# Performance work log

Hardware: AMD Instinct MI355X
Metric: run time of the kernel (lower is better)

The kernel has to match this reference:

```python
import jax, jax.numpy as jnp
import numpy as np

N_HEADS = 12
NEG_INF = -1e9


def rotate_half(x):
    x1, x2 = jnp.split(x, 2, axis=-1)
    return jnp.concatenate((-x2, x1), axis=-1)


def rope_tables(T, D, dtype):
    # matches RotaryEmbedding buffers: emb = cat(freqs, freqs), shape [1,1,T,D]
    inv_freq = 1.0 / (10000.0 ** (jnp.arange(0, D, 2, dtype=jnp.float32) / D))
    t = jnp.arange(T, dtype=jnp.float32)
    freqs = jnp.einsum('i,j->ij', t, inv_freq)
    emb = jnp.concatenate((freqs, freqs), axis=-1)
    return jnp.cos(emb)[None, None].astype(dtype), jnp.sin(emb)[None, None].astype(dtype)


def setup_inputs() -> dict:
    key = jax.random.key(0)
    ks = jax.random.split(key, 5)
    B, T, C = 4, 2048, 768
    s = 1.0 / np.sqrt(C)
    x = jax.random.normal(ks[0], (B, T, C), dtype=jnp.float32)
    wq = jax.random.normal(ks[1], (C, C), dtype=jnp.float32) * s
    wk = jax.random.normal(ks[2], (C, C), dtype=jnp.float32) * s
    wv = jax.random.normal(ks[3], (C, C), dtype=jnp.float32) * s
    wo = jax.random.normal(ks[4], (C, C), dtype=jnp.float32) * s
    causal = jnp.tril(jnp.ones((T, T), dtype=bool))
    mask = jnp.where(causal, 0.0, NEG_INF).astype(jnp.float32)[None, None]
    return {"x": x, "wq": wq, "wk": wk, "wv": wv, "wo": wo, "mask": mask}


def reference(x, wq, wk, wv, wo, mask):
    B, T, C = x.shape
    H = N_HEADS
    D = C // H
    # QKV projections (no bias), reshape to [B,H,T,D]
    def proj(w):
        return (x @ w).reshape(B, T, H, D).transpose(0, 2, 1, 3)
    q, k, v = proj(wq), proj(wk), proj(wv)
    cos, sin = rope_tables(T, D, x.dtype)
    q = q * cos + rotate_half(q) * sin
    k = k * cos + rotate_half(k) * sin
    attn = jnp.einsum('bhqd,bhkd->bhqk', q, k) / jnp.sqrt(jnp.asarray(D, x.dtype))
    attn = attn + mask
    attn = jax.nn.softmax(attn, axis=-1)  # dropout = identity (eval mode)
    out = jnp.einsum('bhqk,bhkd->bhqd', attn, v)
    out = out.transpose(0, 2, 1, 3).reshape(B, T, C)
    return out @ wo
```

## Files before the change

kernel.cpp:

```cpp
#include <hip/hip_runtime.h>
#include <hip/hip_bf16.h>
#include <cmath>

typedef _Float16 f16x8 __attribute__((ext_vector_type(8)));
typedef float f32x4 __attribute__((ext_vector_type(4)));

#define T_SEQ 2048
#define C_DIM 768
#define H_NUM 12
#define NX (8192 * 768)
#define NW (768 * 768)

__device__ __forceinline__ unsigned short f2h(float f) {
    _Float16 h = (_Float16)f;
    return __builtin_bit_cast(unsigned short, h);
}

__device__ __forceinline__ float fexp2(float x) {
#if __has_builtin(__builtin_amdgcn_exp2f)
    return __builtin_amdgcn_exp2f(x);
#else
    return exp2f(x);
#endif
}

__device__ __forceinline__ unsigned int pkrtz(float a, float b) {
    auto r = __builtin_amdgcn_cvt_pkrtz(a, b);
    return __builtin_bit_cast(unsigned int, r);
}

__device__ __forceinline__ unsigned int permlo(unsigned int d0, unsigned int d1) {
#if __has_builtin(__builtin_amdgcn_perm)
    return __builtin_amdgcn_perm(d1, d0, 0x05040100u);
#else
    return (d0 & 0xffffu) | (d1 << 16);
#endif
}
__device__ __forceinline__ unsigned int permhi(unsigned int d0, unsigned int d1) {
#if __has_builtin(__builtin_amdgcn_perm)
    return __builtin_amdgcn_perm(d1, d0, 0x07060302u);
#else
    return (d0 >> 16) | (d1 & 0xffff0000u);
#endif
}

__device__ __forceinline__ void gld16(const unsigned short* g, unsigned short* l) {
    __builtin_amdgcn_global_load_lds(
        (const __attribute__((address_space(1))) unsigned int*)g,
        (__attribute__((address_space(3))) unsigned int*)l, 16, 0, 0);
}

__global__ __launch_bounds__(256)
void prep(const float* __restrict__ x,
          const float* __restrict__ w0, const float* __restrict__ w1,
          const float* __restrict__ w2, const float* __restrict__ w3,
          unsigned short* __restrict__ xb, unsigned short* __restrict__ wt) {
    __shared__ float T[64][65];
    const int pid = blockIdx.x;
    if (pid < 3072) {
        int cidx = pid * 256 + threadIdx.x;
        int row = cidx / 96;
        int cp = cidx - row * 96;
        int dchunk = row * 96 + (cp & ~3) + ((cp & 3) ^ (row & 3));
        const float* s = x + (size_t)cidx * 8;
        float4 v0 = *(const float4*)s, v1 = *(const float4*)(s + 4);
        ushort4 a, b;
        a.x = f2h(v0.x); a.y = f2h(v0.y); a.z = f2h(v0.z); a.w = f2h(v0.w);
        b.x = f2h(v1.x); b.y = f2h(v1.y); b.z = f2h(v1.z); b.w = f2h(v1.w);
        unsigned short* d = xb + (size_t)dchunk * 8;
        *(ushort4*)d = a;
        *(ushort4*)(d + 4) = b;
    } else {
        int t = pid - 3072;
        int z = t / 144, r = t - z * 144;
        int kx = r / 12, ny = r - kx * 12;
        const float* src = (z == 0) ? w0 : (z == 1) ? w1 : (z == 2) ? w2 : w3;
        unsigned short* dst = wt + (size_t)z * NW;
        const int k0 = kx * 64, n0 = ny * 64;
        const int tid = threadIdx.x;
        {
            int rowb = tid >> 4, c4 = (tid & 15) * 4;
#pragma unroll
            for (int i = 0; i < 4; ++i) {
                int row = rowb + i * 16;
                float4 v = *(const float4*)&src[(size_t)(k0 + row) * C_DIM + n0 + c4];
                T[row][c4] = v.x; T[row][c4 + 1] = v.y; T[row][c4 + 2] = v.z; T[row][c4 + 3] = v.w;
            }
        }
        __syncthreads();
        {
            int n = tid & 63, kseg = (tid >> 6) * 16;
            int n_glob = n0 + n;
            unsigned short tmp[16];
#pragma unroll
            for (int j = 0; j < 16; ++j) tmp[j] = f2h(T[kseg + j][n]);
            int base = k0 + (kseg & 32);
            int sub = (kseg >> 3) & 3;
            unsigned short* drow = dst + (size_t)n_glob * C_DIM + base;
            *(uint4*)&drow[(sub ^ (n_glob & 3)) << 3]       = *(uint4*)&tmp[0];
            *(uint4*)&drow[((sub + 1) ^ (n_glob & 3)) << 3] = *(uint4*)&tmp[8];
        }
    }
}

__global__ __launch_bounds__(256, 4)
void qkv_gemm(const unsigned short* __restrict__ xb,
              const unsigned short* __restrict__ wt,
              unsigned short* __restrict__ q_ws,
              unsigned short* __restrict__ k_ws,
              unsigned short* __restrict__ vt_ws) {
    const int pid = blockIdx.x;
    const int xcd = pid & 7, idx = pid >> 3;
    const int mloc = idx / 18, nw = idx - mloc * 18;
    const int which = nw % 3, nx = nw / 3;
    const unsigned short* W = wt + (size_t)which * NW;
    const int n0 = nx * 128, m0 = (xcd * 8 + mloc) * 128;

    __shared__ __align__(16) unsigned short As[8192];
    __shared__ __align__(16) unsigned short Bs[8192];

    const int tid = threadIdx.x, lane = tid & 63, w = tid >> 6;
    const int quad = lane >> 4, l16 = lane & 15;
    const int wm = (w >> 1) * 64, wn = (w & 1) * 64;

    f32x4 acc[4][4] = {};

    for (int k0 = 0; k0 < C_DIM; k0 += 64) {
        __syncthreads();
#pragma unroll
        for (int c = 0; c < 4; ++c) {
            int e = c * 256 + tid;
            int p = e >> 9, row = (e >> 2) & 127, ch = e & 3;
            int kc = k0 + p * 32 + ch * 8;
            gld16(xb + (size_t)(m0 + row) * C_DIM + kc, &As[e * 8]);
            gld16(W  + (size_t)(n0 + row) * C_DIM + kc, &Bs[e * 8]);
        }
        __syncthreads();
#pragma unroll
        for (int p = 0; p < 2; ++p) {
            f16x8 af[4], bf[4];
#pragma unroll
            for (int mt = 0; mt < 4; ++mt) {
                int r = wm + mt * 16 + l16;
                af[mt] = *(const f16x8*)&As[p * 4096 + r * 32 + ((quad ^ (r & 3)) << 3)];
            }
#pragma unroll
            for (int nt = 0; nt < 4; ++nt) {
                int r = wn + nt * 16 + l16;
                bf[nt] = *(const f16x8*)&Bs[p * 4096 + r * 32 + ((quad ^ (r & 3)) << 3)];
            }
#pragma unroll
            for (int mt = 0; mt < 4; ++mt)
#pragma unroll
                for (int nt = 0; nt < 4; ++nt)
                    acc[mt][nt] = __builtin_amdgcn_mfma_f32_16x16x32_f16(af[mt], bf[nt], acc[mt][nt], 0, 0, 0);
        }
    }

    const int head = nx * 2 + (w & 1);

    if (which < 2) {
        unsigned short* dst = (which == 0) ? q_ws : k_ws;
        const float qscale = 0.18033688011112042f;
#pragma unroll
        for (int ntp = 0; ntp < 2; ++ntp) {
            int d1 = ntp * 16 + l16;
            float invf = __expf(-0.28782313662425572f * (float)d1);
#pragma unroll
            for (int mt = 0; mt < 4; ++mt)
#pragma unroll
                for (int reg = 0; reg < 4; ++reg) {
                    int m = m0 + wm + mt * 16 + quad * 4 + reg;
                    int t = m & (T_SEQ - 1), bb = m >> 11;
                    float sn, cs;
                    __sincosf((float)t * invf, &sn, &cs);
                    float v1 = acc[mt][ntp][reg], v2 = acc[mt][ntp + 2][reg];
                    float o1 = v1 * cs - v2 * sn;
                    float o2 = v2 * cs + v1 * sn;
                    if (which == 0) { o1 *= qscale; o2 *= qscale; }
                    size_t o = ((size_t)(bb * H_NUM + head) * T_SEQ + t) * 64 + d1;
                    dst[o] = f2h(o1);
                    dst[o + 32] = f2h(o2);
                }
        }
    } else {
#pragma unroll
        for (int nt = 0; nt < 4; ++nt) {
            int d = nt * 16 + l16;
#pragma unroll
            for (int mt = 0; mt < 4; ++mt) {
                int m = m0 + wm + mt * 16 + quad * 4;
                int t = m & (T_SEQ - 1), bb = m >> 11;
                ushort4 pk;
                pk.x = f2h(acc[mt][nt][0]); pk.y = f2h(acc[mt][nt][1]);
                pk.z = f2h(acc[mt][nt][2]); pk.w = f2h(acc[mt][nt][3]);
                *(ushort4*)&vt_ws[((size_t)(bb * H_NUM + head) * 64 + d) * T_SEQ + t] = pk;
            }
        }
    }
}

__global__ __launch_bounds__(256, 3)
void flash_attn(const unsigned short* __restrict__ q_ws,
                const unsigned short* __restrict__ k_ws,
                const unsigned short* __restrict__ vt_ws,
                unsigned short* __restrict__ attn_out) {
    __shared__ __align__(16) unsigned short Kbuf[2][64 * 64];
    __shared__ __align__(16) unsigned int Ps32[4][16 * 64];

    const int pid = blockIdx.x;
    const int xcd = pid & 7, slot = pid >> 3;
    const int bh_l = slot >> 4;
    const int bh = xcd * 6 + bh_l;
    const int pr = (slot + 3 * bh_l) & 15;
    const int qa = pr, qb = 31 - pr;
    const int b = bh / H_NUM, h = bh % H_NUM;

    const int tid = threadIdx.x, lane = tid & 63, w = tid >> 6;
    const int quad = lane >> 4, l16 = lane & 15;
    const size_t base = (size_t)bh * (T_SEQ * 64);

    const unsigned short* qAp = q_ws + base + (size_t)(qa * 64 + w * 16 + l16) * 64 + quad * 8;
    f16x8 aqA0 = *(const f16x8*)(qAp);
    f16x8 aqA1 = *(const f16x8*)(qAp + 32);
    const unsigned short* qBp = q_ws + base + (size_t)(qb * 64 + w * 16 + l16) * 64 + quad * 8;
    f16x8 aqB0 = *(const f16x8*)(qBp);
    f16x8 aqB1 = *(const f16x8*)(qBp + 32);

    f32x4 accA[4] = {}, accB[4] = {};
    f32x4 laccA = {}, laccB = {};
    f16x8 onesf;
#pragma unroll
    for (int i = 0; i < 8; ++i) onesf[i] = (_Float16)1.0f;

    unsigned int* pw = &Ps32[w][0];

    const int r_in = lane >> 3;
    const int cpr = lane & 7;
    const int gch = (cpr ^ r_in) * 8;

#define DMA_K(P, KT)                                                                   \
    {                                                                                  \
        _Pragma("unroll")                                                              \
        for (int j = 0; j < 2; ++j) {                                                  \
            int row = w * 16 + j * 8 + r_in;                                           \
            gld16(k_ws + base + (size_t)((KT) * 64 + row) * 64 + gch,                  \
                  &Kbuf[P][(w * 16 + j * 8) * 64]);                                    \
        }                                                                              \
    }

    const int fo = (quad ^ (l16 & 7)) << 3;

    const unsigned short* vrow = vt_ws + base + (size_t)l16 * T_SEQ + quad * 8;

    const int wg = (quad & 1) * 4;
    const int l16q = l16 >> 2, l16m = l16 & 3;
    const int s7 = l16 & 7;
    const int rA = l16 * 64;
    const int rp0a = rA + (((2 * quad) ^ s7) << 2);
    const int rp0b = rA + (((2 * quad + 1) ^ s7) << 2);

    DMA_K(0, 0);
    for (int kt = 0; kt <= qb; ++kt) {
        const int cur = kt & 1;
        __syncthreads();
        if (kt < qb) DMA_K(cur ^ 1, kt + 1);
        const int doA = (kt <= qa);

        f16x8 bv[4][2];
#pragma unroll
        for (int nt = 0; nt < 4; ++nt) {
            const unsigned short* vp = vrow + (size_t)nt * 16 * T_SEQ + kt * 64;
            bv[nt][0] = *(const f16x8*)(vp);
            bv[nt][1] = *(const f16x8*)(vp + 32);
        }

        f16x8 bk[4][2];
#pragma unroll
        for (int nt = 0; nt < 4; ++nt) {
            const unsigned short* kr = &Kbuf[cur][(nt * 16 + l16) * 64 + fo];
            bk[nt][0] = *(const f16x8*)(kr);
            bk[nt][1] = *(const f16x8*)((const unsigned short*)((size_t)kr ^ 64));
        }

        f32x4 sB[4] = {}, sA[4] = {};
        __builtin_amdgcn_s_setprio(1);
#pragma unroll
        for (int nt = 0; nt < 4; ++nt) {
            sB[nt] = __builtin_amdgcn_mfma_f32_16x16x32_f16(aqB0, bk[nt][0], sB[nt], 0, 0, 0);
            sB[nt] = __builtin_amdgcn_mfma_f32_16x16x32_f16(aqB1, bk[nt][1], sB[nt], 0, 0, 0);
        }
        if (doA) {
#pragma unroll
            for (int nt = 0; nt < 4; ++nt) {
                sA[nt] = __builtin_amdgcn_mfma_f32_16x16x32_f16(aqA0, bk[nt][0], sA[nt], 0, 0, 0);
                sA[nt] = __builtin_amdgcn_mfma_f32_16x16x32_f16(aqA1, bk[nt][1], sA[nt], 0, 0, 0);
            }
        }
        __builtin_amdgcn_s_setprio(0);
        if (kt == qb) {
#pragma unroll
            for (int nt = 0; nt < 4; ++nt)
#pragma unroll
                for (int reg = 0; reg < 4; ++reg)
                    if (nt * 16 + l16 > w * 16 + quad * 4 + reg) sB[nt][reg] = -1e30f;
        }
        if (kt == qa) {
#pragma unroll
            for (int nt = 0; nt < 4; ++nt)
#pragma unroll
                for (int reg = 0; reg < 4; ++reg)
                    if (nt * 16 + l16 > w * 16 + quad * 4 + reg) sA[nt][reg] = -1e30f;
        }

        if (doA) {
#pragma unroll
            for (int nt = 0; nt < 4; ++nt)
#pragma unroll
                for (int reg = 0; reg < 4; ++reg) {
                    float pB = fexp2(sB[nt][reg]);
                    float pA = fexp2(sA[nt][reg]);
                    pw[(quad * 4 + reg) * 64 + ((((nt * 4) | l16q) ^ (wg | reg)) << 2) + l16m] = pkrtz(pB, pA);
                }
        } else {
#pragma unroll
            for (int nt = 0; nt < 4; ++nt)
#pragma unroll
                for (int reg = 0; reg < 4; ++reg) {
                    float pB = fexp2(sB[nt][reg]);
                    pw[(quad * 4 + reg) * 64 + ((((nt * 4) | l16q) ^ (wg | reg)) << 2) + l16m] = pkrtz(pB, pB);
                }
        }

        uint4 c0 = *(const uint4*)(pw + rp0a);
        uint4 c1 = *(const uint4*)(pw + rp0b);
        uint4 c2 = *(const uint4*)(pw + rp0a + 32);
        uint4 c3 = *(const uint4*)(pw + rp0b + 32);

        uint4 lo0 = { permlo(c0.x, c0.y), permlo(c0.z, c0.w), permlo(c1.x, c1.y), permlo(c1.z, c1.w) };
        uint4 lo1 = { permlo(c2.x, c2.y), permlo(c2.z, c2.w), permlo(c3.x, c3.y), permlo(c3.z, c3.w) };
        f16x8 apB0 = __builtin_bit_cast(f16x8, lo0);
        f16x8 apB1 = __builtin_bit_cast(f16x8, lo1);
        __builtin_amdgcn_s_setprio(1);
#pragma unroll
        for (int nt = 0; nt < 4; ++nt) {
            accB[nt] = __builtin_amdgcn_mfma_f32_16x16x32_f16(apB0, bv[nt][0], accB[nt], 0, 0, 0);
            accB[nt] = __builtin_amdgcn_mfma_f32_16x16x32_f16(apB1, bv[nt][1], accB[nt], 0, 0, 0);
        }
        laccB = __builtin_amdgcn_mfma_f32_16x16x32_f16(apB0, onesf, laccB, 0, 0, 0);
        laccB = __builtin_amdgcn_mfma_f32_16x16x32_f16(apB1, onesf, laccB, 0, 0, 0);
        __builtin_amdgcn_s_setprio(0);
        if (doA) {
            uint4 hi0 = { permhi(c0.x, c0.y), permhi(c0.z, c0.w), permhi(c1.x, c1.y), permhi(c1.z, c1.w) };
            uint4 hi1 = { permhi(c2.x, c2.y), permhi(c2.z, c2.w), permhi(c3.x, c3.y), permhi(c3.z, c3.w) };
            f16x8 apA0 = __builtin_bit_cast(f16x8, hi0);
            f16x8 apA1 = __builtin_bit_cast(f16x8, hi1);
            __builtin_amdgcn_s_setprio(1);
#pragma unroll
            for (int nt = 0; nt < 4; ++nt) {
                accA[nt] = __builtin_amdgcn_mfma_f32_16x16x32_f16(apA0, bv[nt][0], accA[nt], 0, 0, 0);
                accA[nt] = __builtin_amdgcn_mfma_f32_16x16x32_f16(apA1, bv[nt][1], accA[nt], 0, 0, 0);
            }
            laccA = __builtin_amdgcn_mfma_f32_16x16x32_f16(apA0, onesf, laccA, 0, 0, 0);
            laccA = __builtin_amdgcn_mfma_f32_16x16x32_f16(apA1, onesf, laccA, 0, 0, 0);
            __builtin_amdgcn_s_setprio(0);
        }
    }
#undef DMA_K

    float lB[4], lA[4];
#pragma unroll
    for (int reg = 0; reg < 4; ++reg) {
        lB[reg] = 1.0f / laccB[reg];
        lA[reg] = 1.0f / laccA[reg];
    }
#pragma unroll
    for (int nt = 0; nt < 4; ++nt)
#pragma unroll
        for (int reg = 0; reg < 4; ++reg) {
            int col = h * 64 + nt * 16 + l16;
            int tB = qb * 64 + w * 16 + quad * 4 + reg;
            attn_out[(size_t)(b * T_SEQ + tB) * C_DIM + col] = f2h(accB[nt][reg] * lB[reg]);
            int tA = qa * 64 + w * 16 + quad * 4 + reg;
            attn_out[(size_t)(b * T_SEQ + tA) * C_DIM + col] = f2h(accA[nt][reg] * lA[reg]);
        }
}

__global__ __launch_bounds__(256, 3)
void out_proj(const unsigned short* __restrict__ ab,
              const unsigned short* __restrict__ wt_o,
              float* __restrict__ out) {
    const int pid = blockIdx.x;
    const int xcd = pid & 7, idx = pid >> 3;
    const int mloc = idx / 6, nx = idx - mloc * 6;
    const int n0 = nx * 128, m0 = (xcd * 8 + mloc) * 128;

    __shared__ __align__(16) unsigned short As[8192];
    __shared__ __align__(16) unsigned short Bs[8192];

    const int tid = threadIdx.x, lane = tid & 63, w = tid >> 6;
    const int quad = lane >> 4, l16 = lane & 15;
    const int wm = (w >> 1) * 64, wn = (w & 1) * 64;

    f32x4 acc[4][4] = {};
    const int srow = tid >> 1, shalf = tid & 1;

    for (int k0 = 0; k0 < C_DIM; k0 += 64) {
        __syncthreads();
#pragma unroll
        for (int p = 0; p < 2; ++p) {
            const unsigned short* g = ab + (size_t)(m0 + srow) * C_DIM + k0 + p * 32 + shalf * 16;
            uint4 d0 = *(const uint4*)g;
            uint4 d1 = *(const uint4*)(g + 8);
            *(uint4*)&As[p * 4096 + srow * 32 + (((shalf * 2 + 0) ^ (srow & 3)) << 3)] = d0;
            *(uint4*)&As[p * 4096 + srow * 32 + (((shalf * 2 + 1) ^ (srow & 3)) << 3)] = d1;
        }
#pragma unroll
        for (int c = 0; c < 4; ++c) {
            int e = c * 256 + tid;
            int p = e >> 9, row = (e >> 2) & 127, ch = e & 3;
            gld16(wt_o + (size_t)(n0 + row) * C_DIM + k0 + p * 32 + ch * 8, &Bs[e * 8]);
        }
        __syncthreads();
#pragma unroll
        for (int p = 0; p < 2; ++p) {
            f16x8 af[4], bf[4];
#pragma unroll
            for (int mt = 0; mt < 4; ++mt) {
                int r = wm + mt * 16 + l16;
                af[mt] = *(const f16x8*)&As[p * 4096 + r * 32 + ((quad ^ (r & 3)) << 3)];
            }
#pragma unroll
            for (int nt = 0; nt < 4; ++nt) {
                int r = wn + nt * 16 + l16;
                bf[nt] = *(const f16x8*)&Bs[p * 4096 + r * 32 + ((quad ^ (r & 3)) << 3)];
            }
#pragma unroll
            for (int mt = 0; mt < 4; ++mt)
#pragma unroll
                for (int nt = 0; nt < 4; ++nt)
                    acc[mt][nt] = __builtin_amdgcn_mfma_f32_16x16x32_f16(af[mt], bf[nt], acc[mt][nt], 0, 0, 0);
        }
    }

#pragma unroll
    for (int mt = 0; mt < 4; ++mt)
#pragma unroll
        for (int nt = 0; nt < 4; ++nt)
#pragma unroll
            for (int reg = 0; reg < 4; ++reg) {
                int m = m0 + wm + mt * 16 + quad * 4 + reg;
                int n = n0 + wn + nt * 16 + l16;
                out[(size_t)m * C_DIM + n] = acc[mt][nt][reg];
            }
}

extern "C" void kernel_launch(void* const* d_in, const int* in_sizes, int n_in,
                              void* d_out, int out_size, void* d_ws, size_t ws_size,
                              hipStream_t stream) {
    const float* x  = (const float*)d_in[0];
    const float* wq = (const float*)d_in[1];
    const float* wk = (const float*)d_in[2];
    const float* wv = (const float*)d_in[3];
    const float* wo = (const float*)d_in[4];
    float* out = (float*)d_out;

    unsigned short* xb    = (unsigned short*)d_ws;
    unsigned short* wt    = xb + NX;
    unsigned short* q_ws  = wt + 4 * (size_t)NW;
    unsigned short* k_ws  = q_ws + NX;
    unsigned short* vt_ws = k_ws + NX;
    unsigned short* attn  = xb;

    prep<<<3648, 256, 0, stream>>>(x, wq, wk, wv, wo, xb, wt);
    qkv_gemm<<<1152, 256, 0, stream>>>(xb, wt, q_ws, k_ws, vt_ws);
    flash_attn<<<768, 256, 0, stream>>>(q_ws, k_ws, vt_ws, attn);
    out_proj<<<384, 256, 0, stream>>>(attn, wt + 3 * (size_t)NW, out);
}
```

Before: 256.5 us.

## Load K directly from global into registers with software prefetch, dropping LDS staging

Removes the shared-memory double-buffered K tile, its async DMA and the per-iteration __syncthreads. K and V fragments now go straight from global memory into registers, and the loads for the next tile are issued right after the current tile's QK and PV MFMAs so they overlap compute. This removes block-wide barriers and LDS traffic. In exchange, each wave fetches K from global or L2 on its own with no sharing across the block, and register pressure rises, which may hurt occupancy at launch_bounds 3.

```diff
diff --git a/kernel.cpp b/kernel.cpp
--- a/kernel.cpp
+++ b/kernel.cpp
@@ -205,7 +205,6 @@
                 const unsigned short* __restrict__ k_ws,
                 const unsigned short* __restrict__ vt_ws,
                 unsigned short* __restrict__ attn_out) {
-    __shared__ __align__(16) unsigned short Kbuf[2][64 * 64];
     __shared__ __align__(16) unsigned int Ps32[4][16 * 64];
 
     const int pid = blockIdx.x;
@@ -235,23 +234,8 @@
 
     unsigned int* pw = &Ps32[w][0];
 
-    const int r_in = lane >> 3;
-    const int cpr = lane & 7;
-    const int gch = (cpr ^ r_in) * 8;
-
-#define DMA_K(P, KT)                                                                   \
-    {                                                                                  \
-        _Pragma("unroll")                                                              \
-        for (int j = 0; j < 2; ++j) {                                                  \
-            int row = w * 16 + j * 8 + r_in;                                           \
-            gld16(k_ws + base + (size_t)((KT) * 64 + row) * 64 + gch,                  \
-                  &Kbuf[P][(w * 16 + j * 8) * 64]);                                    \
-        }                                                                              \
-    }
-
-    const int fo = (quad ^ (l16 & 7)) << 3;
-
-    const unsigned short* vrow = vt_ws + base + (size_t)l16 * T_SEQ + quad * 8;
+    const unsigned short* kl = k_ws + base + (size_t)l16 * 64 + quad * 8;
+    const unsigned short* vl = vt_ws + base + (size_t)l16 * T_SEQ + quad * 8;
 
     const int wg = (quad & 1) * 4;
     const int l16q = l16 >> 2, l16m = l16 & 3;
@@ -260,28 +244,19 @@
     const int rp0a = rA + (((2 * quad) ^ s7) << 2);
     const int rp0b = rA + (((2 * quad + 1) ^ s7) << 2);
 
-    DMA_K(0, 0);
+    f16x8 bk[4][2], bv[4][2];
+#pragma unroll
+    for (int nt = 0; nt < 4; ++nt) {
+        const unsigned short* kp = kl + (size_t)(nt * 16) * 64;
+        bk[nt][0] = *(const f16x8*)(kp);
+        bk[nt][1] = *(const f16x8*)(kp + 32);
+        const unsigned short* vp = vl + (size_t)(nt * 16) * T_SEQ;
+        bv[nt][0] = *(const f16x8*)(vp);
+        bv[nt][1] = *(const f16x8*)(vp + 32);
+    }
+
     for (int kt = 0; kt <= qb; ++kt) {
-        const int cur = kt & 1;
-        __syncthreads();
-        if (kt < qb) DMA_K(cur ^ 1, kt + 1);
         const int doA = (kt <= qa);
-
-        f16x8 bv[4][2];
-#pragma unroll
-        for (int nt = 0; nt < 4; ++nt) {
-            const unsigned short* vp = vrow + (size_t)nt * 16 * T_SEQ + kt * 64;
-            bv[nt][0] = *(const f16x8*)(vp);
-            bv[nt][1] = *(const f16x8*)(vp + 32);
-        }
-
-        f16x8 bk[4][2];
-#pragma unroll
-        for (int nt = 0; nt < 4; ++nt) {
-            const unsigned short* kr = &Kbuf[cur][(nt * 16 + l16) * 64 + fo];
-            bk[nt][0] = *(const f16x8*)(kr);
-            bk[nt][1] = *(const f16x8*)((const unsigned short*)((size_t)kr ^ 64));
-        }
 
         f32x4 sB[4] = {}, sA[4] = {};
         __builtin_amdgcn_s_setprio(1);
@@ -298,6 +273,16 @@
             }
         }
         __builtin_amdgcn_s_setprio(0);
+
+        if (kt < qb) {
+#pragma unroll
+            for (int nt = 0; nt < 4; ++nt) {
+                const unsigned short* kp = kl + (size_t)((kt + 1) * 64 + nt * 16) * 64;
+                bk[nt][0] = *(const f16x8*)(kp);
+                bk[nt][1] = *(const f16x8*)(kp + 32);
+            }
+        }
+
         if (kt == qb) {
 #pragma unroll
             for (int nt = 0; nt < 4; ++nt)
@@ -365,8 +350,16 @@
             laccA = __builtin_amdgcn_mfma_f32_16x16x32_f16(apA1, onesf, laccA, 0, 0, 0);
             __builtin_amdgcn_s_setprio(0);
         }
-    }
-#undef DMA_K
+
+        if (kt < qb) {
+#pragma unroll
+            for (int nt = 0; nt < 4; ++nt) {
+                const unsigned short* vp = vl + (size_t)(nt * 16) * T_SEQ + (kt + 1) * 64;
+                bv[nt][0] = *(const f16x8*)(vp);
+                bv[nt][1] = *(const f16x8*)(vp + 32);
+            }
+        }
+    }
 
     float lB[4], lA[4];
 #pragma unroll
```

Result: slower. 324.4 us (+26.5%).
